# Optimization experiments

Hardware: AMD Instinct MI355X
Metric: run time of the kernel (lower is better)

## Reference

```python
import jax, jax.numpy as jnp
import numpy as np
import math

HIDDEN = 32
N_NODES = 4096
N_EDGES = 8192
FEAT = HIDDEN * 16
# e3nn FullyConnectedTensorProduct instruction order: loop i_in1, i_in2, i_out
PATHS = [(l1, l2, l3) for l1 in range(4) for l2 in range(4) for l3 in range(4)
         if abs(l1 - l2) <= l3 <= l1 + l2 and (l1 + l2 + l3) % 2 == 0]
WEIGHT_NUMEL = len(PATHS) * HIDDEN * HIDDEN  # 23 * 1024 = 23552
_CNT = {l3: sum(1 for p in PATHS if p[2] == l3) for l3 in range(4)}
# path_weight: irrep_normalization='component', path_normalization='element'
PATH_W = {p: math.sqrt((2 * p[2] + 1) / (_CNT[p[2]] * HIDDEN)) for p in PATHS}


def _sh(xp, x, y, z):
    # e3nn-convention real spherical harmonics l=0..3, 'component' normalization.
    # Assumes unit-norm (x,y,z). xp is np or jnp.
    s3, s5, s7, s15 = math.sqrt(3.), math.sqrt(5.), math.sqrt(7.), math.sqrt(15.)
    c58, c38 = math.sqrt(5. / 8.), math.sqrt(3. / 8.)
    comps = [
        xp.ones_like(x),
        s3 * x, s3 * y, s3 * z,
        s5 * s3 * x * z, s5 * s3 * x * y, s5 * (y * y - 0.5 * (x * x + z * z)),
        s5 * s3 * y * z, s5 * (s3 / 2.) * (z * z - x * x),
        s7 * c58 * x * (3. * z * z - x * x), s7 * s15 * x * y * z,
        s7 * c38 * x * (5. * y * y - 1.), s7 * 0.5 * y * (5. * y * y - 3.),
        s7 * c38 * z * (5. * y * y - 1.), s7 * (s15 / 2.) * y * (z * z - x * x),
        s7 * c58 * z * (z * z - 3. * x * x),
    ]
    return xp.stack(comps, axis=-1)


def _wigner_tables():
    # Real-basis unit-Frobenius invariant tensors (e3nn wigner_3j up to sign),
    # computed as Gaunt integrals of the real SH over the sphere (exact quadrature:
    # integrand degree <= 9, Gauss-Legendre x uniform phi).
    nu, nphi = 16, 32
    u, wu = np.polynomial.legendre.leggauss(nu)
    phi = np.arange(nphi) * (2.0 * np.pi / nphi)
    uu = np.repeat(u, nphi)
    ww = np.repeat(wu, nphi) * (2.0 * np.pi / nphi)
    pp = np.tile(phi, nu)
    st = np.sqrt(np.maximum(1.0 - uu * uu, 0.0))
    Y = _sh(np, st * np.cos(pp), st * np.sin(pp), uu)  # [P,16]
    tabs = {}
    for key in set(PATHS):
        l1, l2, l3 = key
        C = np.einsum('p,pi,pj,pk->ijk', ww,
                      Y[:, l1 * l1:(l1 + 1) ** 2],
                      Y[:, l2 * l2:(l2 + 1) ** 2],
                      Y[:, l3 * l3:(l3 + 1) ** 2])
        tabs[key] = (C / np.linalg.norm(C)).astype(np.float32)
    return tabs


W3J = _wigner_tables()


def setup_inputs():
    key = jax.random.key(0)
    k1, k2, k3, k4, k5 = jax.random.split(key, 5)
    return {
        'node_features': jax.random.normal(k1, (N_NODES, FEAT), jnp.float32),
        'edge_index': jax.random.randint(k2, (2, N_EDGES), 0, N_NODES),
        'edge_vectors': jax.random.normal(k3, (N_EDGES, 3), jnp.float32),
        'w_weight': jax.random.uniform(k4, (WEIGHT_NUMEL, 1), jnp.float32, -1.0, 1.0),
        'w_bias': jax.random.uniform(k5, (WEIGHT_NUMEL,), jnp.float32, -1.0, 1.0),
    }


def reference(node_features, edge_index, edge_vectors, w_weight, w_bias):
    src, dst = edge_index[0], edge_index[1]
    N = node_features.shape[0]
    E = edge_vectors.shape[0]
    lengths = jnp.maximum(jnp.linalg.norm(edge_vectors, axis=-1, keepdims=True), 1e-8)
    unit = edge_vectors / lengths
    Y = _sh(jnp, unit[:, 0], unit[:, 1], unit[:, 2])            # [E,16]
    # weight_net: Linear(1, weight_numel)
    W = lengths * w_weight[:, 0][None, :] + w_bias[None, :]     # [E,23552]
    x_src = node_features[src]                                  # [E,512] gather
    acc = [jnp.zeros((E, HIDDEN, 2 * l + 1), node_features.dtype) for l in range(4)]
    for p_idx, (l1, l2, l3) in enumerate(PATHS):
        x1 = x_src[:, HIDDEN * l1 * l1: HIDDEN * (l1 + 1) ** 2].reshape(E, HIDDEN, 2 * l1 + 1)
        y2 = Y[:, l2 * l2:(l2 + 1) ** 2]                        # [E,2l2+1]
        C = jnp.asarray(W3J[(l1, l2, l3)])                      # [2l1+1,2l2+1,2l3+1]
        wp = W[:, p_idx * HIDDEN * HIDDEN:(p_idx + 1) * HIDDEN * HIDDEN].reshape(E, HIDDEN, HIDDEN)
        tmp = jnp.einsum('eui,ej,ijk->euk', x1, y2, C)
        acc[l3] = acc[l3] + PATH_W[(l1, l2, l3)] * jnp.einsum('euk,euw->ewk', tmp, wp)
    messages = jnp.concatenate([a.reshape(E, -1) for a in acc], axis=-1)  # [E,512]
    return jax.ops.segment_sum(messages, dst, num_segments=N)
```

## Files before the change

### kernel.cpp

```cpp
#include <hip/hip_runtime.h>
#include <math.h>

#define N_PATHS 23
#define HIDDEN  32
#define N_NODES 4096
#define N_EDGES 8192
#define FEAT    512
#define BLK     128
#define ZERO_BLOCKS 256

#define WAVE_SYNC() asm volatile("s_waitcnt lgkmcnt(0)" ::: "memory")

typedef __attribute__((ext_vector_type(8))) short bf16x8;
typedef __attribute__((ext_vector_type(4))) float f32x4;

constexpr int cL1[N_PATHS] = {0,0,0,0, 1,1,1,1,1,1, 2,2,2,2,2,2,2, 3,3,3,3,3,3};
constexpr int cL2[N_PATHS] = {0,1,2,3, 0,1,1,2,2,3, 0,1,1,2,2,3,3, 0,1,2,2,3,3};
constexpr int cL3[N_PATHS] = {0,1,2,3, 1,0,2,1,3,2, 2,1,3,0,2,1,3, 3,2,1,3,0,2};
constexpr int cCOFF[N_PATHS]= {0,1,10,35,84,93,102,147,192,297,402,427,472,577,602,727,832,1077,1126,1231,1336,1581,1630};
constexpr int cL3P[N_PATHS] = {0,5,13,21, 1,4,7,11,15,19, 2,6,9,10,14,18,22, 3,8,12,16,17,20};
constexpr int cL3S[5] = {0,4,10,17,23};
constexpr int cOFF3[4] = {0,32,128,288};
__device__ const int CNT_L3[4] = {4,6,7,6};
__device__ const int D_L3[N_PATHS] = {0,1,2,3, 1,0,2,1,3,2, 2,1,3,0,2,1,3, 3,2,1,3,0,2};

__device__ const double GLX8[8] = {
    -0.96028985649753623168, -0.79666647741362673959, -0.52553240991632898582, -0.18343464249564980494,
     0.18343464249564980494,  0.52553240991632898582,  0.79666647741362673959,  0.96028985649753623168};
__device__ const double GLW8[8] = {
     0.10122853629037625915,  0.22238103445337447054,  0.31370664587788728734,  0.36268378337836198297,
     0.36268378337836198297,  0.31370664587788728734,  0.22238103445337447054,  0.10122853629037625915};
__device__ const double COSP16[16] = {
  1.0,                     0.92387953251128675613,  0.70710678118654752440,  0.38268343236508977173,
  0.0,                    -0.38268343236508977173, -0.70710678118654752440, -0.92387953251128675613,
 -1.0,                    -0.92387953251128675613, -0.70710678118654752440, -0.38268343236508977173,
  0.0,                     0.38268343236508977173,  0.70710678118654752440,  0.92387953251128675613};
__device__ const double SINP16[16] = {
  0.0,                     0.38268343236508977173,  0.70710678118654752440,  0.92387953251128675613,
  1.0,                     0.92387953251128675613,  0.70710678118654752440,  0.38268343236508977173,
  0.0,                    -0.38268343236508977173, -0.70710678118654752440, -0.92387953251128675613,
 -1.0,                    -0.92387953251128675613, -0.70710678118654752440, -0.38268343236508977173};

__device__ inline void sh_f64(double x, double y, double z, double* Y) {
    const double s3 = 1.7320508075688772935, s5 = 2.2360679774997896964,
                 s7 = 2.6457513110645905905, s15 = 3.8729833462074168852;
    const double c58 = 0.79056941504209483300, c38 = 0.61237243569579452455;
    Y[0] = 1.0;
    Y[1] = s3*x;  Y[2] = s3*y;  Y[3] = s3*z;
    Y[4] = s5*s3*x*z;  Y[5] = s5*s3*x*y;
    Y[6] = s5*(y*y - 0.5*(x*x + z*z));
    Y[7] = s5*s3*y*z;  Y[8] = s5*(s3/2.0)*(z*z - x*x);
    Y[9] = s7*c58*x*(3.0*z*z - x*x);
    Y[10]= s7*s15*x*y*z;
    Y[11]= s7*c38*x*(5.0*y*y - 1.0);
    Y[12]= s7*0.5*y*(5.0*y*y - 3.0);
    Y[13]= s7*c38*z*(5.0*y*y - 1.0);
    Y[14]= s7*(s15/2.0)*y*(z*z - x*x);
    Y[15]= s7*c58*z*(z*z - 3.0*x*x);
}

__device__ inline void sh_f32(float x, float y, float z, float* Y) {
    const float s3 = 1.73205080757f, s5 = 2.23606797750f, s7 = 2.64575131106f, s15 = 3.87298334621f;
    const float c58 = 0.79056941504f, c38 = 0.61237243570f;
    Y[0] = 1.0f;
    Y[1] = s3*x;  Y[2] = s3*y;  Y[3] = s3*z;
    Y[4] = s15*x*z;  Y[5] = s15*x*y;
    Y[6] = s5*(y*y - 0.5f*(x*x + z*z));
    Y[7] = s15*y*z;  Y[8] = s5*(s3*0.5f)*(z*z - x*x);
    Y[9] = s7*c58*x*(3.0f*z*z - x*x);
    Y[10]= s7*s15*x*y*z;
    Y[11]= s7*c38*x*(5.0f*y*y - 1.0f);
    Y[12]= s7*0.5f*y*(5.0f*y*y - 3.0f);
    Y[13]= s7*c38*z*(5.0f*y*y - 1.0f);
    Y[14]= s7*(s15*0.5f)*y*(z*z - x*x);
    Y[15]= s7*c58*z*(z*z - 3.0f*x*x);
}

__device__ inline unsigned short bf16rne(float x) {
    unsigned int u = __float_as_uint(x);
    unsigned int r = (u + 0x7FFFu + ((u >> 16) & 1u)) >> 16;
    return (unsigned short)r;
}
__device__ inline float bf16f(unsigned short h) {
    return __uint_as_float(((unsigned int)h) << 16);
}

__global__ __launch_bounds__(512) void w3j_setup_kernel(
    const float* __restrict__ ww, const float* __restrict__ wb,
    float* __restrict__ g_w3j,
    unsigned short* __restrict__ Awhi, unsigned short* __restrict__ Awlo,
    unsigned short* __restrict__ Abhi, unsigned short* __restrict__ Ablo,
    float* __restrict__ out) {
    const int t = threadIdx.x;

    if (blockIdx.x >= N_PATHS) {
        const int b = blockIdx.x - N_PATHS;
        float4* o4 = (float4*)(out + (size_t)b * (N_NODES*FEAT/ZERO_BLOCKS));
#pragma unroll
        for (int r = 0; r < 4; ++r)
            o4[t + 512*r] = make_float4(0.f,0.f,0.f,0.f);
        return;
    }

    __shared__ float s_Yq[128][17];
    __shared__ float s_wq[128];
    __shared__ float s_part[256];
    __shared__ float red[256];
    __shared__ float s_scale;

    const int p = blockIdx.x;
    const int l1 = cL1[p], l2 = cL2[p];
    const int l3 = D_L3[p];
    const int d2 = 2*l2+1, d3 = 2*l3+1;
    const int csize = (2*l1+1)*d2*d3;
    const double step = 2.0*3.14159265358979323846/16.0;

#pragma unroll
    for (int r = 0; r < 2; ++r) {
        const int idx = t + 512*r;
        const int w = idx >> 5, u = idx & 31;
        const float vw = ww[p*1024 + u*32 + w];
        const float vb = wb[p*1024 + u*32 + w];
        const unsigned short hw = bf16rne(vw);
        const unsigned short hb = bf16rne(vb);
        const int o = p*1024 + w*32 + u;
        Awhi[o] = hw;  Awlo[o] = bf16rne(vw - bf16f(hw));
        Abhi[o] = hb;  Ablo[o] = bf16rne(vb - bf16f(hb));
    }

    if (t < 128) {
        const int iu = t >> 4, ip = t & 15;
        const double u = GLX8[iu];
        const double st = sqrt(fmax(1.0 - u*u, 0.0));
        double Y[16];
        sh_f64(st*COSP16[ip], st*SINP16[ip], u, Y);
#pragma unroll
        for (int i = 0; i < 16; ++i) s_Yq[t][i] = (float)Y[i];
        s_wq[t] = (float)(GLW8[iu] * step);
    }
    __syncthreads();

    const int entry0 = t >> 2, sub = t & 3;
#pragma unroll
    for (int pass = 0; pass < 2; ++pass) {
        const int entry = entry0 + pass*128;
        float acc = 0.f;
        if (entry < csize) {
            const int i = entry/(d2*d3); const int r = entry - i*(d2*d3);
            const int j = r/d3; const int k = r - j*d3;
            const int ai = l1*l1+i, bi = l2*l2+j, ci = l3*l3+k;
#pragma unroll 4
            for (int it = 0; it < 32; ++it) {
                const int q = it*4 + sub;
                acc = fmaf(s_wq[q] * s_Yq[q][ai] * s_Yq[q][bi], s_Yq[q][ci], acc);
            }
        }
        acc += __shfl_xor(acc, 1);
        acc += __shfl_xor(acc, 2);
        if (sub == 0 && entry < csize) s_part[entry] = acc;
    }
    __syncthreads();

    if (t < 256) { const float v = (t < csize) ? s_part[t] : 0.f; red[t] = v*v; }
    __syncthreads();
    for (int s = 128; s > 0; s >>= 1) {
        if (t < s) red[t] += red[t+s];
        __syncthreads();
    }
    if (t == 0) {
        const float pw = sqrtf((float)(2*l3+1) / ((float)CNT_L3[l3] * (float)HIDDEN));
        s_scale = pw / sqrtf(red[0]);
    }
    __syncthreads();
    if (t < csize) g_w3j[cCOFF[p] + t] = s_part[t] * s_scale;
}

template<int G, int P>
__device__ __forceinline__ void do_path(
    int lane, int u, int el, int bvaddr, int avaddr,
    const float (&xr)[16],
    const float* __restrict__ w3j,
    const unsigned short* __restrict__ Awhi, const unsigned short* __restrict__ Awlo,
    const unsigned short* __restrict__ Abhi, const unsigned short* __restrict__ Ablo,
    const float* sY, float* sz,
    unsigned short* sbh, unsigned short* sbl,
    f32x4 (&Cw)[2], f32x4 (&Cb)[2])
{
    constexpr int l1 = cL1[P], l2 = cL2[P];
    constexpr int d1 = 2*l1+1, d2 = 2*l2+1, d3 = 2*G+1;
    constexpr int zc = d1*d3;
    constexpr int xo = l1*l1;

#pragma unroll
    for (int base = 0; base < 2*zc; base += 64) {
        const int idx = base + lane;
        if (idx < 2*zc) {
            const int elz = (idx >= zc) ? 1 : 0;
            const int r = idx - elz*zc;
            const int i = r / d3, k = r - i*d3;
            const float* Cp = w3j + cCOFF[P] + i*(d2*d3) + k;
            const float* Yp = sY + elz*16 + l2*l2;
            float acc = 0.f;
#pragma unroll
            for (int j = 0; j < d2; ++j) acc = fmaf(Yp[j], Cp[j*d3], acc);
            sz[elz*49 + r] = acc;
        }
    }
    WAVE_SYNC();

    {
        const float* zr = sz + el*49;
        unsigned short* bh = sbh + el*(d3*40) + u;
        unsigned short* bl = sbl + el*(d3*40) + u;
#pragma unroll
        for (int k = 0; k < d3; ++k) {
            float tv = 0.f;
#pragma unroll
            for (int i = 0; i < d1; ++i) tv = fmaf(xr[xo+i], zr[i*d3+k], tv);
            const unsigned int tb = __float_as_uint(tv);
            const float lof = tv - __uint_as_float(tb & 0xFFFF0000u);
            bh[k*40] = (unsigned short)(tb >> 16);
            bl[k*40] = (unsigned short)(__float_as_uint(lof) >> 16);
        }
    }
    WAVE_SYNC();

    const unsigned short* pwh = Awhi + P*1024;
    const unsigned short* pwl = Awlo + P*1024;
    const unsigned short* pbh = Abhi + P*1024;
    const unsigned short* pbl = Ablo + P*1024;
    bf16x8 awh[2], awl[2], abh[2], abl[2];
#pragma unroll
    for (int mt = 0; mt < 2; ++mt) {
        awh[mt] = *(const bf16x8*)(pwh + mt*512 + avaddr);
        awl[mt] = *(const bf16x8*)(pwl + mt*512 + avaddr);
        abh[mt] = *(const bf16x8*)(pbh + mt*512 + avaddr);
        abl[mt] = *(const bf16x8*)(pbl + mt*512 + avaddr);
    }
    const bf16x8 bh = *(const bf16x8*)(sbh + bvaddr);
    const bf16x8 bl = *(const bf16x8*)(sbl + bvaddr);
#pragma unroll
    for (int mt = 0; mt < 2; ++mt) {
        Cw[mt] = __builtin_amdgcn_mfma_f32_16x16x32_bf16(awh[mt], bh, Cw[mt], 0, 0, 0);
        Cw[mt] = __builtin_amdgcn_mfma_f32_16x16x32_bf16(awh[mt], bl, Cw[mt], 0, 0, 0);
        Cw[mt] = __builtin_amdgcn_mfma_f32_16x16x32_bf16(awl[mt], bh, Cw[mt], 0, 0, 0);
        Cb[mt] = __builtin_amdgcn_mfma_f32_16x16x32_bf16(abh[mt], bh, Cb[mt], 0, 0, 0);
        Cb[mt] = __builtin_amdgcn_mfma_f32_16x16x32_bf16(abh[mt], bl, Cb[mt], 0, 0, 0);
        Cb[mt] = __builtin_amdgcn_mfma_f32_16x16x32_bf16(abl[mt], bh, Cb[mt], 0, 0, 0);
    }
    WAVE_SYNC();
}

template<int G>
__device__ __forceinline__ void do_group(
    int lane, int u, int el, int ln, int lq, int bvaddr, int avaddr,
    const float (&xr)[16],
    const float* __restrict__ w3j,
    const unsigned short* __restrict__ Awhi, const unsigned short* __restrict__ Awlo,
    const unsigned short* __restrict__ Abhi, const unsigned short* __restrict__ Ablo,
    const float* sY, float* sz,
    unsigned short* sbh, unsigned short* sbl,
    const float* slen, float* smsg)
{
    constexpr int d3 = 2*G+1;
    constexpr int s = cL3S[G];
    constexpr int n = cL3S[G+1] - cL3S[G];
    f32x4 Cw[2], Cb[2];
#pragma unroll
    for (int mt = 0; mt < 2; ++mt) {
        Cw[mt] = (f32x4){0.f,0.f,0.f,0.f};
        Cb[mt] = (f32x4){0.f,0.f,0.f,0.f};
    }

    do_path<G, cL3P[s+0]>(lane,u,el,bvaddr,avaddr,xr,w3j,Awhi,Awlo,Abhi,Ablo,sY,sz,sbh,sbl,Cw,Cb);
    do_path<G, cL3P[s+1]>(lane,u,el,bvaddr,avaddr,xr,w3j,Awhi,Awlo,Abhi,Ablo,sY,sz,sbh,sbl,Cw,Cb);
    do_path<G, cL3P[s+2]>(lane,u,el,bvaddr,avaddr,xr,w3j,Awhi,Awlo,Abhi,Ablo,sY,sz,sbh,sbl,Cw,Cb);
    do_path<G, cL3P[s+3]>(lane,u,el,bvaddr,avaddr,xr,w3j,Awhi,Awlo,Abhi,Ablo,sY,sz,sbh,sbl,Cw,Cb);
    if constexpr (n > 4)
        do_path<G, cL3P[s+4]>(lane,u,el,bvaddr,avaddr,xr,w3j,Awhi,Awlo,Abhi,Ablo,sY,sz,sbh,sbl,Cw,Cb);
    if constexpr (n > 5)
        do_path<G, cL3P[s+5]>(lane,u,el,bvaddr,avaddr,xr,w3j,Awhi,Awlo,Abhi,Ablo,sY,sz,sbh,sbl,Cw,Cb);
    if constexpr (n > 6)
        do_path<G, cL3P[s+6]>(lane,u,el,bvaddr,avaddr,xr,w3j,Awhi,Awlo,Abhi,Ablo,sY,sz,sbh,sbl,Cw,Cb);

    if (ln < 2*d3) {
        const int elc = ln / d3, k = ln - elc*d3;
        const float len = slen[elc];
        float* mp = smsg + elc*FEAT + cOFF3[G] + k;
#pragma unroll
        for (int mt = 0; mt < 2; ++mt)
#pragma unroll
            for (int r = 0; r < 4; ++r)
                mp[(mt*16 + lq*4 + r)*d3] = fmaf(len, Cw[mt][r], Cb[mt][r]);
    }
}

__global__ __launch_bounds__(BLK, 4) void edge_kernel(
    const float* __restrict__ nf,
    const int*   __restrict__ eidx,
    const float* __restrict__ ev,
    const float* __restrict__ w3j,
    const unsigned short* __restrict__ Awhi,
    const unsigned short* __restrict__ Awlo,
    const unsigned short* __restrict__ Abhi,
    const unsigned short* __restrict__ Ablo,
    float*       __restrict__ out)
{
    __shared__ float s_zp[2][2*49];
    __shared__ float s_Y[2][32];
    __shared__ float s_len[2][2];
    __shared__ int   s_src[2][2];
    __shared__ int   s_dst[2][2];
    __shared__ __align__(16) unsigned short s_Bhi[2][640];
    __shared__ __align__(16) unsigned short s_Blo[2][640];
    __shared__ float s_msg[2][2*FEAT];

    const int t    = threadIdx.x;
    const int wave = t >> 6;
    const int lane = t & 63;
    const int ln   = lane & 15;
    const int lq   = lane >> 4;
    const int u    = lane & 31;
    const int el   = lane >> 5;
    const int e0   = blockIdx.x * 4 + wave*2;
    const int bvaddr = ln*40 + lq*8;
    const int avaddr = ln*32 + lq*8;

    if (lane < 2) {
        const int e = e0 + lane;
        s_src[wave][lane] = eidx[e];
        s_dst[wave][lane] = eidx[N_EDGES + e];
        const float x = ev[e*3+0], y = ev[e*3+1], z = ev[e*3+2];
        const float len = sqrtf(x*x + y*y + z*z);
        const float lc = fmaxf(len, 1e-8f);
        s_len[wave][lane] = lc;
        float Yl[16];
        sh_f32(x/lc, y/lc, z/lc, Yl);
#pragma unroll
        for (int i = 0; i < 16; ++i) s_Y[wave][lane*16+i] = Yl[i];
    }
    WAVE_SYNC();

    float xr[16];
    {
        const float* xrow = nf + (size_t)s_src[wave][el]*FEAT;
        xr[0] = xrow[u];
#pragma unroll
        for (int i = 0; i < 3; ++i) xr[1+i] = xrow[32 + u*3 + i];
#pragma unroll
        for (int i = 0; i < 5; ++i) xr[4+i] = xrow[128 + u*5 + i];
#pragma unroll
        for (int i = 0; i < 7; ++i) xr[9+i] = xrow[288 + u*7 + i];
    }

    do_group<0>(lane,u,el,ln,lq,bvaddr,avaddr,xr,w3j,Awhi,Awlo,Abhi,Ablo,
                s_Y[wave], s_zp[wave], s_Bhi[wave], s_Blo[wave], s_len[wave], s_msg[wave]);
    do_group<1>(lane,u,el,ln,lq,bvaddr,avaddr,xr,w3j,Awhi,Awlo,Abhi,Ablo,
                s_Y[wave], s_zp[wave], s_Bhi[wave], s_Blo[wave], s_len[wave], s_msg[wave]);
    do_group<2>(lane,u,el,ln,lq,bvaddr,avaddr,xr,w3j,Awhi,Awlo,Abhi,Ablo,
                s_Y[wave], s_zp[wave], s_Bhi[wave], s_Blo[wave], s_len[wave], s_msg[wave]);
    do_group<3>(lane,u,el,ln,lq,bvaddr,avaddr,xr,w3j,Awhi,Awlo,Abhi,Ablo,
                s_Y[wave], s_zp[wave], s_Bhi[wave], s_Blo[wave], s_len[wave], s_msg[wave]);
    WAVE_SYNC();

    for (int i = lane; i < 2*FEAT; i += 64) {
        const int elc = i >> 9, m = i & 511;
        atomicAdd(&out[(size_t)s_dst[wave][elc]*FEAT + m], s_msg[wave][i]);
    }
}

extern "C" void kernel_launch(void* const* d_in, const int* in_sizes, int n_in,
                              void* d_out, int out_size, void* d_ws, size_t ws_size,
                              hipStream_t stream) {
    const float* nf   = (const float*)d_in[0];
    const int*   eidx = (const int*)  d_in[1];
    const float* ev   = (const float*)d_in[2];
    const float* ww   = (const float*)d_in[3];
    const float* wb   = (const float*)d_in[4];
    float* out = (float*)d_out;

    float* w3j = (float*)d_ws;
    unsigned short* Awhi = (unsigned short*)((char*)d_ws + 16384);
    unsigned short* Awlo = Awhi + N_PATHS*1024;
    unsigned short* Abhi = Awlo + N_PATHS*1024;
    unsigned short* Ablo = Abhi + N_PATHS*1024;

    w3j_setup_kernel<<<N_PATHS + ZERO_BLOCKS, 512, 0, stream>>>(
        ww, wb, w3j, Awhi, Awlo, Abhi, Ablo, out);
    edge_kernel<<<N_EDGES/4, BLK, 0, stream>>>(nf, eidx, ev, w3j, Awhi, Awlo, Abhi, Ablo, out);
}
```

Before: 141.8 us.

## Process four edges per wave with 32x32x16 MFMA tiles

Each wave now handles four edges instead of two. The small 16x16x32 MFMAs are replaced with 32x32x16 MFMAs whose N dimension spans the four edges' output components, and each lane computes two channels of the intermediate tensor product. The A-operand weight fragments are loaded before the B-fragment build so their latency can overlap it. The intent is to amortise the per-path weight loads and MFMA issue over more edges and halve the block count. The cost is more registers, since the launch_bounds occupancy hint is dropped, and more LDS per block.

Measured after the change: 121.4 us. 1.17x faster.

```diff
diff --git a/kernel.cpp b/kernel.cpp
--- a/kernel.cpp
+++ b/kernel.cpp
@@ -11,12 +11,11 @@
 
 #define WAVE_SYNC() asm volatile("s_waitcnt lgkmcnt(0)" ::: "memory")
 
-typedef __attribute__((ext_vector_type(8))) short bf16x8;
-typedef __attribute__((ext_vector_type(4))) float f32x4;
+typedef __attribute__((ext_vector_type(8)))  short bf16x8;
+typedef __attribute__((ext_vector_type(16))) float f32x16;
 
 constexpr int cL1[N_PATHS] = {0,0,0,0, 1,1,1,1,1,1, 2,2,2,2,2,2,2, 3,3,3,3,3,3};
 constexpr int cL2[N_PATHS] = {0,1,2,3, 0,1,1,2,2,3, 0,1,1,2,2,3,3, 0,1,2,2,3,3};
-constexpr int cL3[N_PATHS] = {0,1,2,3, 1,0,2,1,3,2, 2,1,3,0,2,1,3, 3,2,1,3,0,2};
 constexpr int cCOFF[N_PATHS]= {0,1,10,35,84,93,102,147,192,297,402,427,472,577,602,727,832,1077,1126,1231,1336,1581,1630};
 constexpr int cL3P[N_PATHS] = {0,5,13,21, 1,4,7,11,15,19, 2,6,9,10,14,18,22, 3,8,12,16,17,20};
 constexpr int cL3S[5] = {0,4,10,17,23};
@@ -177,14 +176,14 @@
 
 template<int G, int P>
 __device__ __forceinline__ void do_path(
-    int lane, int u, int el, int bvaddr, int avaddr,
-    const float (&xr)[16],
+    int lane, int el4, int u0, int bvaddr, int avaddr,
+    const float (&xr0)[16], const float (&xr1)[16],
     const float* __restrict__ w3j,
     const unsigned short* __restrict__ Awhi, const unsigned short* __restrict__ Awlo,
     const unsigned short* __restrict__ Abhi, const unsigned short* __restrict__ Ablo,
     const float* sY, float* sz,
     unsigned short* sbh, unsigned short* sbl,
-    f32x4 (&Cw)[2], f32x4 (&Cb)[2])
+    f32x16 &Cw, f32x16 &Cb)
 {
     constexpr int l1 = cL1[P], l2 = cL2[P];
     constexpr int d1 = 2*l1+1, d2 = 2*l2+1, d3 = 2*G+1;
@@ -192,10 +191,10 @@
     constexpr int xo = l1*l1;
 
 #pragma unroll
-    for (int base = 0; base < 2*zc; base += 64) {
+    for (int base = 0; base < 4*zc; base += 64) {
         const int idx = base + lane;
-        if (idx < 2*zc) {
-            const int elz = (idx >= zc) ? 1 : 0;
+        if (idx < 4*zc) {
+            const int elz = idx / zc;
             const int r = idx - elz*zc;
             const int i = r / d3, k = r - i*d3;
             const float* Cp = w3j + cCOFF[P] + i*(d2*d3) + k;
@@ -203,24 +202,7 @@
             float acc = 0.f;
 #pragma unroll
             for (int j = 0; j < d2; ++j) acc = fmaf(Yp[j], Cp[j*d3], acc);
-            sz[elz*49 + r] = acc;
-        }
-    }
-    WAVE_SYNC();
-
-    {
-        const float* zr = sz + el*49;
-        unsigned short* bh = sbh + el*(d3*40) + u;
-        unsigned short* bl = sbl + el*(d3*40) + u;
-#pragma unroll
-        for (int k = 0; k < d3; ++k) {
-            float tv = 0.f;
-#pragma unroll
-            for (int i = 0; i < d1; ++i) tv = fmaf(xr[xo+i], zr[i*d3+k], tv);
-            const unsigned int tb = __float_as_uint(tv);
-            const float lof = tv - __uint_as_float(tb & 0xFFFF0000u);
-            bh[k*40] = (unsigned short)(tb >> 16);
-            bl[k*40] = (unsigned short)(__float_as_uint(lof) >> 16);
+            sz[elz*50 + r] = acc;
         }
     }
     WAVE_SYNC();
@@ -231,30 +213,54 @@
     const unsigned short* pbl = Ablo + P*1024;
     bf16x8 awh[2], awl[2], abh[2], abl[2];
 #pragma unroll
-    for (int mt = 0; mt < 2; ++mt) {
-        awh[mt] = *(const bf16x8*)(pwh + mt*512 + avaddr);
-        awl[mt] = *(const bf16x8*)(pwl + mt*512 + avaddr);
-        abh[mt] = *(const bf16x8*)(pbh + mt*512 + avaddr);
-        abl[mt] = *(const bf16x8*)(pbl + mt*512 + avaddr);
-    }
-    const bf16x8 bh = *(const bf16x8*)(sbh + bvaddr);
-    const bf16x8 bl = *(const bf16x8*)(sbl + bvaddr);
-#pragma unroll
-    for (int mt = 0; mt < 2; ++mt) {
-        Cw[mt] = __builtin_amdgcn_mfma_f32_16x16x32_bf16(awh[mt], bh, Cw[mt], 0, 0, 0);
-        Cw[mt] = __builtin_amdgcn_mfma_f32_16x16x32_bf16(awh[mt], bl, Cw[mt], 0, 0, 0);
-        Cw[mt] = __builtin_amdgcn_mfma_f32_16x16x32_bf16(awl[mt], bh, Cw[mt], 0, 0, 0);
-        Cb[mt] = __builtin_amdgcn_mfma_f32_16x16x32_bf16(abh[mt], bh, Cb[mt], 0, 0, 0);
-        Cb[mt] = __builtin_amdgcn_mfma_f32_16x16x32_bf16(abh[mt], bl, Cb[mt], 0, 0, 0);
-        Cb[mt] = __builtin_amdgcn_mfma_f32_16x16x32_bf16(abl[mt], bh, Cb[mt], 0, 0, 0);
+    for (int kc = 0; kc < 2; ++kc) {
+        awh[kc] = *(const bf16x8*)(pwh + avaddr + kc*16);
+        awl[kc] = *(const bf16x8*)(pwl + avaddr + kc*16);
+        abh[kc] = *(const bf16x8*)(pbh + avaddr + kc*16);
+        abl[kc] = *(const bf16x8*)(pbl + avaddr + kc*16);
+    }
+
+    {
+        const float* zr = sz + el4*50;
+        unsigned short* bh = sbh + (el4*d3)*40 + 2*u0;
+        unsigned short* bl = sbl + (el4*d3)*40 + 2*u0;
+#pragma unroll
+        for (int k = 0; k < d3; ++k) {
+            float t0 = 0.f, t1 = 0.f;
+#pragma unroll
+            for (int i = 0; i < d1; ++i) {
+                const float zz = zr[i*d3 + k];
+                t0 = fmaf(xr0[xo+i], zz, t0);
+                t1 = fmaf(xr1[xo+i], zz, t1);
+            }
+            const unsigned int b0 = __float_as_uint(t0);
+            const unsigned int b1 = __float_as_uint(t1);
+            const float l0 = t0 - __uint_as_float(b0 & 0xFFFF0000u);
+            const float l1f = t1 - __uint_as_float(b1 & 0xFFFF0000u);
+            *(unsigned int*)(bh + k*40) = (b0 >> 16) | (b1 & 0xFFFF0000u);
+            *(unsigned int*)(bl + k*40) = (__float_as_uint(l0) >> 16) | (__float_as_uint(l1f) & 0xFFFF0000u);
+        }
+    }
+    WAVE_SYNC();
+
+#pragma unroll
+    for (int kc = 0; kc < 2; ++kc) {
+        const bf16x8 bh = *(const bf16x8*)(sbh + bvaddr + kc*16);
+        const bf16x8 bl = *(const bf16x8*)(sbl + bvaddr + kc*16);
+        Cw = __builtin_amdgcn_mfma_f32_32x32x16_bf16(awh[kc], bh, Cw, 0, 0, 0);
+        Cb = __builtin_amdgcn_mfma_f32_32x32x16_bf16(abh[kc], bh, Cb, 0, 0, 0);
+        Cw = __builtin_amdgcn_mfma_f32_32x32x16_bf16(awh[kc], bl, Cw, 0, 0, 0);
+        Cb = __builtin_amdgcn_mfma_f32_32x32x16_bf16(abh[kc], bl, Cb, 0, 0, 0);
+        Cw = __builtin_amdgcn_mfma_f32_32x32x16_bf16(awl[kc], bh, Cw, 0, 0, 0);
+        Cb = __builtin_amdgcn_mfma_f32_32x32x16_bf16(abl[kc], bh, Cb, 0, 0, 0);
     }
     WAVE_SYNC();
 }
 
 template<int G>
 __device__ __forceinline__ void do_group(
-    int lane, int u, int el, int ln, int lq, int bvaddr, int avaddr,
-    const float (&xr)[16],
+    int lane, int el4, int u0, int bvaddr, int avaddr,
+    const float (&xr0)[16], const float (&xr1)[16],
     const float* __restrict__ w3j,
     const unsigned short* __restrict__ Awhi, const unsigned short* __restrict__ Awlo,
     const unsigned short* __restrict__ Abhi, const unsigned short* __restrict__ Ablo,
@@ -265,37 +271,33 @@
     constexpr int d3 = 2*G+1;
     constexpr int s = cL3S[G];
     constexpr int n = cL3S[G+1] - cL3S[G];
-    f32x4 Cw[2], Cb[2];
-#pragma unroll
-    for (int mt = 0; mt < 2; ++mt) {
-        Cw[mt] = (f32x4){0.f,0.f,0.f,0.f};
-        Cb[mt] = (f32x4){0.f,0.f,0.f,0.f};
-    }
-
-    do_path<G, cL3P[s+0]>(lane,u,el,bvaddr,avaddr,xr,w3j,Awhi,Awlo,Abhi,Ablo,sY,sz,sbh,sbl,Cw,Cb);
-    do_path<G, cL3P[s+1]>(lane,u,el,bvaddr,avaddr,xr,w3j,Awhi,Awlo,Abhi,Ablo,sY,sz,sbh,sbl,Cw,Cb);
-    do_path<G, cL3P[s+2]>(lane,u,el,bvaddr,avaddr,xr,w3j,Awhi,Awlo,Abhi,Ablo,sY,sz,sbh,sbl,Cw,Cb);
-    do_path<G, cL3P[s+3]>(lane,u,el,bvaddr,avaddr,xr,w3j,Awhi,Awlo,Abhi,Ablo,sY,sz,sbh,sbl,Cw,Cb);
+    f32x16 Cw = (f32x16)(0.f), Cb = (f32x16)(0.f);
+
+    do_path<G, cL3P[s+0]>(lane,el4,u0,bvaddr,avaddr,xr0,xr1,w3j,Awhi,Awlo,Abhi,Ablo,sY,sz,sbh,sbl,Cw,Cb);
+    do_path<G, cL3P[s+1]>(lane,el4,u0,bvaddr,avaddr,xr0,xr1,w3j,Awhi,Awlo,Abhi,Ablo,sY,sz,sbh,sbl,Cw,Cb);
+    do_path<G, cL3P[s+2]>(lane,el4,u0,bvaddr,avaddr,xr0,xr1,w3j,Awhi,Awlo,Abhi,Ablo,sY,sz,sbh,sbl,Cw,Cb);
+    do_path<G, cL3P[s+3]>(lane,el4,u0,bvaddr,avaddr,xr0,xr1,w3j,Awhi,Awlo,Abhi,Ablo,sY,sz,sbh,sbl,Cw,Cb);
     if constexpr (n > 4)
-        do_path<G, cL3P[s+4]>(lane,u,el,bvaddr,avaddr,xr,w3j,Awhi,Awlo,Abhi,Ablo,sY,sz,sbh,sbl,Cw,Cb);
+        do_path<G, cL3P[s+4]>(lane,el4,u0,bvaddr,avaddr,xr0,xr1,w3j,Awhi,Awlo,Abhi,Ablo,sY,sz,sbh,sbl,Cw,Cb);
     if constexpr (n > 5)
-        do_path<G, cL3P[s+5]>(lane,u,el,bvaddr,avaddr,xr,w3j,Awhi,Awlo,Abhi,Ablo,sY,sz,sbh,sbl,Cw,Cb);
+        do_path<G, cL3P[s+5]>(lane,el4,u0,bvaddr,avaddr,xr0,xr1,w3j,Awhi,Awlo,Abhi,Ablo,sY,sz,sbh,sbl,Cw,Cb);
     if constexpr (n > 6)
-        do_path<G, cL3P[s+6]>(lane,u,el,bvaddr,avaddr,xr,w3j,Awhi,Awlo,Abhi,Ablo,sY,sz,sbh,sbl,Cw,Cb);
-
-    if (ln < 2*d3) {
-        const int elc = ln / d3, k = ln - elc*d3;
+        do_path<G, cL3P[s+6]>(lane,el4,u0,bvaddr,avaddr,xr0,xr1,w3j,Awhi,Awlo,Abhi,Ablo,sY,sz,sbh,sbl,Cw,Cb);
+
+    const int col = lane & 31;
+    if (col < 4*d3) {
+        const int elc = col / d3, k = col - elc*d3;
         const float len = slen[elc];
         float* mp = smsg + elc*FEAT + cOFF3[G] + k;
 #pragma unroll
-        for (int mt = 0; mt < 2; ++mt)
-#pragma unroll
-            for (int r = 0; r < 4; ++r)
-                mp[(mt*16 + lq*4 + r)*d3] = fmaf(len, Cw[mt][r], Cb[mt][r]);
-    }
-}
-
-__global__ __launch_bounds__(BLK, 4) void edge_kernel(
+        for (int reg = 0; reg < 16; ++reg) {
+            const int w = (reg & 3) + 8*(reg >> 2) + 4*(lane >> 5);
+            mp[w*d3] = fmaf(len, Cw[reg], Cb[reg]);
+        }
+    }
+}
+
+__global__ __launch_bounds__(BLK) void edge_kernel(
     const float* __restrict__ nf,
     const int*   __restrict__ eidx,
     const float* __restrict__ ev,
@@ -306,27 +308,25 @@
     const unsigned short* __restrict__ Ablo,
     float*       __restrict__ out)
 {
-    __shared__ float s_zp[2][2*49];
-    __shared__ float s_Y[2][32];
-    __shared__ float s_len[2][2];
-    __shared__ int   s_src[2][2];
-    __shared__ int   s_dst[2][2];
-    __shared__ __align__(16) unsigned short s_Bhi[2][640];
-    __shared__ __align__(16) unsigned short s_Blo[2][640];
-    __shared__ float s_msg[2][2*FEAT];
+    __shared__ float s_zp[2][200];
+    __shared__ float s_Y[2][64];
+    __shared__ float s_len[2][4];
+    __shared__ int   s_src[2][4];
+    __shared__ int   s_dst[2][4];
+    __shared__ __align__(16) unsigned short s_Bhi[2][1280];
+    __shared__ __align__(16) unsigned short s_Blo[2][1280];
+    __shared__ float s_msg[2][4*FEAT];
 
     const int t    = threadIdx.x;
     const int wave = t >> 6;
     const int lane = t & 63;
-    const int ln   = lane & 15;
-    const int lq   = lane >> 4;
-    const int u    = lane & 31;
-    const int el   = lane >> 5;
-    const int e0   = blockIdx.x * 4 + wave*2;
-    const int bvaddr = ln*40 + lq*8;
-    const int avaddr = ln*32 + lq*8;
-
-    if (lane < 2) {
+    const int el4  = lane >> 4;
+    const int u0   = lane & 15;
+    const int e0   = blockIdx.x * 8 + wave*4;
+    const int bvaddr = (lane & 31)*40 + (lane >> 5)*8;
+    const int avaddr = (lane & 31)*32 + (lane >> 5)*8;
+
+    if (lane < 4) {
         const int e = e0 + lane;
         s_src[wave][lane] = eidx[e];
         s_dst[wave][lane] = eidx[N_EDGES + e];
@@ -341,29 +341,30 @@
     }
     WAVE_SYNC();
 
-    float xr[16];
+    float xr0[16], xr1[16];
     {
-        const float* xrow = nf + (size_t)s_src[wave][el]*FEAT;
-        xr[0] = xrow[u];
-#pragma unroll
-        for (int i = 0; i < 3; ++i) xr[1+i] = xrow[32 + u*3 + i];
-#pragma unroll
-        for (int i = 0; i < 5; ++i) xr[4+i] = xrow[128 + u*5 + i];
-#pragma unroll
-        for (int i = 0; i < 7; ++i) xr[9+i] = xrow[288 + u*7 + i];
-    }
-
-    do_group<0>(lane,u,el,ln,lq,bvaddr,avaddr,xr,w3j,Awhi,Awlo,Abhi,Ablo,
+        const float* xrow = nf + (size_t)s_src[wave][el4]*FEAT;
+        const int ua = 2*u0, ub = 2*u0 + 1;
+        xr0[0] = xrow[ua];                 xr1[0] = xrow[ub];
+#pragma unroll
+        for (int i = 0; i < 3; ++i) { xr0[1+i] = xrow[32 + ua*3 + i];  xr1[1+i] = xrow[32 + ub*3 + i]; }
+#pragma unroll
+        for (int i = 0; i < 5; ++i) { xr0[4+i] = xrow[128 + ua*5 + i]; xr1[4+i] = xrow[128 + ub*5 + i]; }
+#pragma unroll
+        for (int i = 0; i < 7; ++i) { xr0[9+i] = xrow[288 + ua*7 + i]; xr1[9+i] = xrow[288 + ub*7 + i]; }
+    }
+
+    do_group<0>(lane,el4,u0,bvaddr,avaddr,xr0,xr1,w3j,Awhi,Awlo,Abhi,Ablo,
                 s_Y[wave], s_zp[wave], s_Bhi[wave], s_Blo[wave], s_len[wave], s_msg[wave]);
-    do_group<1>(lane,u,el,ln,lq,bvaddr,avaddr,xr,w3j,Awhi,Awlo,Abhi,Ablo,
+    do_group<1>(lane,el4,u0,bvaddr,avaddr,xr0,xr1,w3j,Awhi,Awlo,Abhi,Ablo,
                 s_Y[wave], s_zp[wave], s_Bhi[wave], s_Blo[wave], s_len[wave], s_msg[wave]);
-    do_group<2>(lane,u,el,ln,lq,bvaddr,avaddr,xr,w3j,Awhi,Awlo,Abhi,Ablo,
+    do_group<2>(lane,el4,u0,bvaddr,avaddr,xr0,xr1,w3j,Awhi,Awlo,Abhi,Ablo,
                 s_Y[wave], s_zp[wave], s_Bhi[wave], s_Blo[wave], s_len[wave], s_msg[wave]);
-    do_group<3>(lane,u,el,ln,lq,bvaddr,avaddr,xr,w3j,Awhi,Awlo,Abhi,Ablo,
+    do_group<3>(lane,el4,u0,bvaddr,avaddr,xr0,xr1,w3j,Awhi,Awlo,Abhi,Ablo,
                 s_Y[wave], s_zp[wave], s_Bhi[wave], s_Blo[wave], s_len[wave], s_msg[wave]);
     WAVE_SYNC();
 
-    for (int i = lane; i < 2*FEAT; i += 64) {
+    for (int i = lane; i < 4*FEAT; i += 64) {
         const int elc = i >> 9, m = i & 511;
         atomicAdd(&out[(size_t)s_dst[wave][elc]*FEAT + m], s_msg[wave][i]);
     }
@@ -387,5 +388,5 @@
 
     w3j_setup_kernel<<<N_PATHS + ZERO_BLOCKS, 512, 0, stream>>>(
         ww, wb, w3j, Awhi, Awlo, Abhi, Ablo, out);
-    edge_kernel<<<N_EDGES/4, BLK, 0, stream>>>(nf, eidx, ev, w3j, Awhi, Awlo, Abhi, Ablo, out);
-}
+    edge_kernel<<<N_EDGES/8, BLK, 0, stream>>>(nf, eidx, ev, w3j, Awhi, Awlo, Abhi, Ablo, out);
+}
```
